# Performance work log

Hardware: AMD Instinct MI355X
Metric: run time of the kernel (lower is better)

Reference implementation:

```python
import jax, jax.numpy as jnp
import numpy as np
from jax import lax

B, OBS, E, H = 65536, 20, 64, 64


def setup_inputs() -> dict:
    key = jax.random.key(0)
    ks = jax.random.split(key, 13)
    s = 0.1
    inp = {
        "obs_traj": jax.random.normal(ks[0], (B, OBS, 2), jnp.float32),
        "W_emb": jax.random.normal(ks[1], (E, 2), jnp.float32) * s,
        "b_emb": jax.random.normal(ks[2], (E,), jnp.float32) * s,
        "Wih_e": jax.random.normal(ks[3], (4 * H, E), jnp.float32) * s,
        "Whh_e": jax.random.normal(ks[4], (4 * H, H), jnp.float32) * s,
        "bih_e": jax.random.normal(ks[5], (4 * H,), jnp.float32) * s,
        "bhh_e": jax.random.normal(ks[6], (4 * H,), jnp.float32) * s,
        "Wih_d": jax.random.normal(ks[7], (4 * H, E), jnp.float32) * s,
        "Whh_d": jax.random.normal(ks[8], (4 * H, H), jnp.float32) * s,
        "bih_d": jax.random.normal(ks[9], (4 * H,), jnp.float32) * s,
        "bhh_d": jax.random.normal(ks[10], (4 * H,), jnp.float32) * s,
        "W_fc": jax.random.normal(ks[11], (2, H), jnp.float32) * s,
        "b_fc": jax.random.normal(ks[12], (2,), jnp.float32) * s,
        "pred_len": 12,
    }
    return inp


def _lstm_step(x, h, c, Wih, Whh, b):
    # PyTorch LSTM gate order: i, f, g, o
    g = x @ Wih.T + h @ Whh.T + b  # [B, 4H]
    i, f, gg, o = jnp.split(g, 4, axis=-1)
    c2 = jax.nn.sigmoid(f) * c + jax.nn.sigmoid(i) * jnp.tanh(gg)
    h2 = jax.nn.sigmoid(o) * jnp.tanh(c2)
    return h2, c2


def reference(obs_traj, W_emb, b_emb, Wih_e, Whh_e, bih_e, bhh_e,
              Wih_d, Whh_d, bih_d, bhh_d, W_fc, b_fc, pred_len):
    bsz = obs_traj.shape[0]
    dt = obs_traj.dtype
    # Encoder: embed all observed steps at once, then scan the LSTM over time.
    emb = jax.nn.relu(obs_traj @ W_emb.T + b_emb)  # [B, OBS, E]
    b_e = bih_e + bhh_e
    h0 = jnp.zeros((bsz, H), dt)
    c0 = jnp.zeros((bsz, H), dt)

    def enc_step(carry, x_t):
        h, c = carry
        h, c = _lstm_step(x_t, h, c, Wih_e, Whh_e, b_e)
        return (h, c), None

    (h, c), _ = lax.scan(enc_step, (h0, c0), jnp.swapaxes(emb, 0, 1))

    b_d = bih_d + bhh_d
    dec_in = jax.nn.relu(obs_traj[:, -1, :] @ W_emb.T + b_emb)  # [B, E]

    def dec_step(carry, _):
        h, c, x = carry
        h, c = _lstm_step(x, h, c, Wih_d, Whh_d, b_d)
        pred = h @ W_fc.T + b_fc  # [B, 2]
        nxt = jax.nn.relu(pred @ W_emb.T + b_emb)
        return (h, c, nxt), pred

    _, preds = lax.scan(dec_step, (h, c, dec_in), None, length=pred_len)
    return jnp.swapaxes(preds, 0, 1)  # [B, pred_len, 2]
```

## Files before the change

### kernel.cpp

```cpp
#include <hip/hip_runtime.h>

typedef __bf16 bf16x8 __attribute__((ext_vector_type(8)));
typedef __bf16 bf16x4 __attribute__((ext_vector_type(4)));
typedef float  f32x4  __attribute__((ext_vector_type(4)));
typedef float  f32x2  __attribute__((ext_vector_type(2)));

constexpr int BATCH = 65536;
constexpr int OBS   = 20;
constexpr int PRED  = 12;
constexpr int BT    = 128;
constexpr int AST   = 136;

constexpr float SIO = -1.4426950408889634f;
constexpr float SG  =  2.8853900817779268f;

__device__ __forceinline__ float exp2_(float x) { return __builtin_amdgcn_exp2f(x); }
__device__ __forceinline__ float rcp_(float x)  { return __builtin_amdgcn_rcpf(x); }

struct SmallW {
    float  bcomb_e[256];
    float  bcomb_d[256];
    float4 embc[64];
    float  wfc[128];
    float  bfc[2];
};

__global__ __launch_bounds__(256, 2)
void vanilla_lstm(const float* __restrict__ obs,
                  const float* __restrict__ W_emb, const float* __restrict__ b_emb,
                  const float* __restrict__ Wih_e, const float* __restrict__ Whh_e,
                  const float* __restrict__ bih_e, const float* __restrict__ bhh_e,
                  const float* __restrict__ Wih_d, const float* __restrict__ Whh_d,
                  const float* __restrict__ bih_d, const float* __restrict__ bhh_d,
                  const float* __restrict__ W_fc,  const float* __restrict__ b_fc,
                  float* __restrict__ out)
{
    __shared__ __align__(16) __bf16 As[BT * AST];
    __shared__ __align__(16) float  pred_s[BT * 2];
    __shared__ SmallW sw;

    const int tid  = threadIdx.x;
    const int wv   = tid >> 6;
    const int lane = tid & 63;
    const int m    = lane & 15;
    const int q    = lane >> 4;
    const int wblk = wv * 16;
    const size_t gRow0 = (size_t)blockIdx.x * BT;

    sw.bcomb_e[tid] = bih_e[tid] + bhh_e[tid];
    sw.bcomb_d[tid] = bih_d[tid] + bhh_d[tid];
    if (tid < 64)  sw.embc[tid] = make_float4(W_emb[2 * tid], W_emb[2 * tid + 1], b_emb[tid], 0.f);
    if (tid < 128) sw.wfc[tid]  = W_fc[tid];
    if (tid < 2)   sw.bfc[tid]  = b_fc[tid];

    {
        uint4 z; z.x = z.y = z.z = z.w = 0u;
        uint4* p = (uint4*)As;
        constexpr int NV = BT * AST * 2 / 16;
        #pragma unroll
        for (int i = 0; i < NV / 256; ++i) p[tid + i * 256] = z;
        if (tid < (NV % 256)) p[tid + (NV / 256) * 256] = z;
    }

    bf16x8 bfr[4][4];
    auto load_bfr = [&](const float* Wih, const float* Whh) {
        #pragma unroll
        for (int c = 0; c < 4; ++c) {
            const float sc = (c == 2) ? SG : SIO;
            const int n = c * 64 + wblk + m;
            #pragma unroll
            for (int kt = 0; kt < 4; ++kt) {
                const float* s = (kt < 2) ? (Wih + n * 64 + kt * 32 + q * 8)
                                          : (Whh + n * 64 + (kt - 2) * 32 + q * 8);
                float4 a = *(const float4*)s;
                float4 b = *(const float4*)(s + 4);
                bf16x8 v;
                v[0] = (__bf16)(sc * a.x); v[1] = (__bf16)(sc * a.y);
                v[2] = (__bf16)(sc * a.z); v[3] = (__bf16)(sc * a.w);
                v[4] = (__bf16)(sc * b.x); v[5] = (__bf16)(sc * b.y);
                v[6] = (__bf16)(sc * b.z); v[7] = (__bf16)(sc * b.w);
                bfr[c][kt] = v;
            }
        }
    };
    load_bfr(Wih_e, Whh_e);

    f32x4 cst[8];
    #pragma unroll
    for (int i = 0; i < 8; ++i) cst[i] = f32x4{0.f, 0.f, 0.f, 0.f};

    __syncthreads();

    f32x4 bias4[4];
    auto load_bias = [&](const float* bc) {
        #pragma unroll
        for (int c = 0; c < 4; ++c) {
            const float sc = (c == 2) ? SG : SIO;
            f32x4 b = *(const f32x4*)&bc[c * 64 + wblk + q * 4];
            bias4[c] = f32x4{sc * b[0], sc * b[1], sc * b[2], sc * b[3]};
        }
    };
    load_bias(sw.bcomb_e);

    f32x4 acc[2][2][4];

    auto gemm_sub = [&](int chunk, int half) {
        #pragma unroll
        for (int nt = 0; nt < 2; ++nt)
            #pragma unroll
            for (int c = 0; c < 4; ++c)
                acc[half][nt][c] = bias4[c];
        #pragma unroll
        for (int kt = 0; kt < 4; ++kt) {
            bf16x8 af[2];
            #pragma unroll
            for (int nt = 0; nt < 2; ++nt)
                af[nt] = *(const bf16x8*)&As[(chunk * 64 + (half * 2 + nt) * 16 + m) * AST + kt * 32 + q * 8];
            #pragma unroll
            for (int nt = 0; nt < 2; ++nt)
                #pragma unroll
                for (int c = 0; c < 4; ++c)
                    acc[half][nt][c] = __builtin_amdgcn_mfma_f32_16x16x32_bf16(
                        bfr[c][kt], af[nt], acc[half][nt][c], 0, 0, 0);
        }
    };

    auto update_sub = [&](int chunk, int half) {
        #pragma unroll
        for (int nt = 0; nt < 2; ++nt) {
            const int idx = chunk * 4 + half * 2 + nt;
            const int row = chunk * 64 + (half * 2 + nt) * 16 + m;
            f32x4 ci = cst[idx];
            bf16x4 h4;
            #pragma unroll
            for (int r = 0; r < 4; ++r) {
                const float gi = acc[half][nt][0][r];
                const float gf = acc[half][nt][1][r];
                const float gg = acc[half][nt][2][r];
                const float go = acc[half][nt][3][r];
                const float Ef = exp2_(gf);
                const float a  = ci[r] * rcp_(1.0f + Ef);
                const float Ei = exp2_(gi);
                const float Eg = exp2_(fminf(fmaxf(gg, -80.f), 80.f));
                const float d1 = 1.0f + Ei;
                const float r1 = rcp_(fmaf(d1, Eg, d1));
                const float cN = fmaf(Eg - 1.0f, r1, a);
                const float Eo = exp2_(go);
                const float Ec = exp2_(fminf(fmaxf(cN * SG, -80.f), 80.f));
                const float d2 = 1.0f + Eo;
                const float r2 = rcp_(fmaf(d2, Ec, d2));
                const float h  = (Ec - 1.0f) * r2;
                ci[r] = cN;
                h4[r] = (__bf16)h;
            }
            cst[idx] = ci;
            *(bf16x4*)&As[row * AST + 64 + wblk + q * 4] = h4;
        }
    };

    auto emb_row = [&](int row, float o0, float o1) {
        #pragma unroll
        for (int h8 = 0; h8 < 2; ++h8) {
            bf16x8 v;
            #pragma unroll
            for (int j = 0; j < 8; ++j) {
                float4 wc = sw.embc[wblk + h8 * 8 + j];
                v[j] = (__bf16)fmaxf(fmaf(o0, wc.x, fmaf(o1, wc.y, wc.z)), 0.f);
            }
            *(bf16x8*)&As[row * AST + wblk + h8 * 8] = v;
        }
    };

    const float* obr0 = obs + (gRow0 + lane) * (OBS * 2);
    const float* obr1 = obs + (gRow0 + 64 + lane) * (OBS * 2);

    {
        f32x2 o0 = *(const f32x2*)obr0;
        f32x2 o1 = *(const f32x2*)obr1;
        emb_row(lane, o0[0], o0[1]);
        emb_row(64 + lane, o1[0], o1[1]);
    }
    __syncthreads();
    gemm_sub(0, 0);
    gemm_sub(0, 1);

    for (int t = 0; t < OBS; ++t) {
        __syncthreads();
        f32x2 on0{0.f, 0.f};
        if (t + 1 < OBS) on0 = *(const f32x2*)(obr0 + (t + 1) * 2);
        update_sub(0, 0);
        gemm_sub(1, 0);
        update_sub(0, 1);
        gemm_sub(1, 1);
        if (t + 1 < OBS) emb_row(lane, on0[0], on0[1]);
        __syncthreads();
        f32x2 on1{0.f, 0.f};
        if (t + 1 < OBS) on1 = *(const f32x2*)(obr1 + (t + 1) * 2);
        update_sub(1, 0);
        if (t + 1 < OBS) gemm_sub(0, 0);
        update_sub(1, 1);
        if (t + 1 < OBS) {
            gemm_sub(0, 1);
            emb_row(64 + lane, on1[0], on1[1]);
        }
    }

    load_bfr(Wih_d, Whh_d);
    load_bias(sw.bcomb_d);
    gemm_sub(0, 0);
    gemm_sub(0, 1);

    auto pred_phase = [&](int chunk, int td) {
        const int prow = chunk * 64 + (tid >> 2);
        const int comp = (tid >> 1) & 1, half = tid & 1;
        const int cb = half * 32;
        float p = 0.f;
        #pragma unroll
        for (int e8 = 0; e8 < 4; ++e8) {
            bf16x8 hv = *(const bf16x8*)&As[prow * AST + 64 + cb + e8 * 8];
            f32x4 w0 = *(const f32x4*)&sw.wfc[comp * 64 + cb + e8 * 8];
            f32x4 w1 = *(const f32x4*)&sw.wfc[comp * 64 + cb + e8 * 8 + 4];
            p += (float)hv[0] * w0[0] + (float)hv[1] * w0[1] + (float)hv[2] * w0[2] + (float)hv[3] * w0[3]
               + (float)hv[4] * w1[0] + (float)hv[5] * w1[1] + (float)hv[6] * w1[2] + (float)hv[7] * w1[3];
        }
        p += __shfl_xor(p, 1, 64);
        if (half == 0) {
            p += sw.bfc[comp];
            pred_s[prow * 2 + comp] = p;
            out[((gRow0 + prow) * PRED + td) * 2 + comp] = p;
        }
    };
    auto emb_dec = [&](int chunk) {
        const int row = chunk * 64 + lane;
        f32x2 pv = *(const f32x2*)&pred_s[row * 2];
        emb_row(row, pv[0], pv[1]);
    };

    for (int td = 0; td < PRED; ++td) {
        __syncthreads();
        update_sub(0, 0);
        gemm_sub(1, 0);
        update_sub(0, 1);
        gemm_sub(1, 1);
        __syncthreads();
        update_sub(1, 0);
        update_sub(1, 1);
        pred_phase(0, td);
        __syncthreads();
        pred_phase(1, td);
        if (td + 1 < PRED) emb_dec(0);
        __syncthreads();
        if (td + 1 < PRED) {
            emb_dec(1);
            gemm_sub(0, 0);
            gemm_sub(0, 1);
        }
    }
}

extern "C" void kernel_launch(void* const* d_in, const int* in_sizes, int n_in,
                              void* d_out, int out_size, void* d_ws, size_t ws_size,
                              hipStream_t stream) {
    (void)in_sizes; (void)n_in; (void)d_ws; (void)ws_size; (void)out_size;
    const float* obs   = (const float*)d_in[0];
    const float* W_emb = (const float*)d_in[1];
    const float* b_emb = (const float*)d_in[2];
    const float* Wih_e = (const float*)d_in[3];
    const float* Whh_e = (const float*)d_in[4];
    const float* bih_e = (const float*)d_in[5];
    const float* bhh_e = (const float*)d_in[6];
    const float* Wih_d = (const float*)d_in[7];
    const float* Whh_d = (const float*)d_in[8];
    const float* bih_d = (const float*)d_in[9];
    const float* bhh_d = (const float*)d_in[10];
    const float* W_fc  = (const float*)d_in[11];
    const float* b_fc  = (const float*)d_in[12];
    float* o = (float*)d_out;

    dim3 grid(BATCH / BT), block(256);
    hipLaunchKernelGGL(vanilla_lstm, grid, block, 0, stream,
                       obs, W_emb, b_emb, Wih_e, Whh_e, bih_e, bhh_e,
                       Wih_d, Whh_d, bih_d, bhh_d, W_fc, b_fc, o);
}
```

Before: 285.2 us.

## Halve batch tile to 64 rows and raise occupancy to three blocks per CU

```diff
diff --git a/kernel.cpp b/kernel.cpp
--- a/kernel.cpp
+++ b/kernel.cpp
@@ -8,7 +8,7 @@
 constexpr int BATCH = 65536;
 constexpr int OBS   = 20;
 constexpr int PRED  = 12;
-constexpr int BT    = 128;
+constexpr int BT    = 64;
 constexpr int AST   = 136;
 
 constexpr float SIO = -1.4426950408889634f;
@@ -18,14 +18,14 @@
 __device__ __forceinline__ float rcp_(float x)  { return __builtin_amdgcn_rcpf(x); }
 
 struct SmallW {
-    float  bcomb_e[256];
-    float  bcomb_d[256];
+    float  biasf_e[256];
+    float  biasf_d[256];
     float4 embc[64];
     float  wfc[128];
     float  bfc[2];
 };
 
-__global__ __launch_bounds__(256, 2)
+__global__ __launch_bounds__(256, 3)
 void vanilla_lstm(const float* __restrict__ obs,
                   const float* __restrict__ W_emb, const float* __restrict__ b_emb,
                   const float* __restrict__ Wih_e, const float* __restrict__ Whh_e,
@@ -47,8 +47,13 @@
     const int wblk = wv * 16;
     const size_t gRow0 = (size_t)blockIdx.x * BT;
 
-    sw.bcomb_e[tid] = bih_e[tid] + bhh_e[tid];
-    sw.bcomb_d[tid] = bih_d[tid] + bhh_d[tid];
+    {
+        const int wv_ = tid >> 6, c_ = (tid >> 4) & 3, qr = tid & 15;
+        const int g = c_ * 64 + wv_ * 16 + qr;
+        const float sc = (c_ == 2) ? SG : SIO;
+        sw.biasf_e[tid] = sc * (bih_e[g] + bhh_e[g]);
+        sw.biasf_d[tid] = sc * (bih_d[g] + bhh_d[g]);
+    }
     if (tid < 64)  sw.embc[tid] = make_float4(W_emb[2 * tid], W_emb[2 * tid + 1], b_emb[tid], 0.f);
     if (tid < 128) sw.wfc[tid]  = W_fc[tid];
     if (tid < 2)   sw.bfc[tid]  = b_fc[tid];
@@ -85,68 +90,58 @@
     };
     load_bfr(Wih_e, Whh_e);
 
-    f32x4 cst[8];
+    f32x4 cst[4];
     #pragma unroll
-    for (int i = 0; i < 8; ++i) cst[i] = f32x4{0.f, 0.f, 0.f, 0.f};
+    for (int i = 0; i < 4; ++i) cst[i] = f32x4{0.f, 0.f, 0.f, 0.f};
 
     __syncthreads();
 
-    f32x4 bias4[4];
-    auto load_bias = [&](const float* bc) {
+    f32x4 acc[2][2][4];
+
+    auto gemm = [&](int chunk, const float* bfrag) {
         #pragma unroll
         for (int c = 0; c < 4; ++c) {
-            const float sc = (c == 2) ? SG : SIO;
-            f32x4 b = *(const f32x4*)&bc[c * 64 + wblk + q * 4];
-            bias4[c] = f32x4{sc * b[0], sc * b[1], sc * b[2], sc * b[3]};
-        }
-    };
-    load_bias(sw.bcomb_e);
-
-    f32x4 acc[2][2][4];
-
-    auto gemm_sub = [&](int chunk, int half) {
-        #pragma unroll
-        for (int nt = 0; nt < 2; ++nt)
-            #pragma unroll
-            for (int c = 0; c < 4; ++c)
-                acc[half][nt][c] = bias4[c];
+            f32x4 b = *(const f32x4*)&bfrag[(wv * 4 + c) * 16 + q * 4];
+            acc[chunk][0][c] = b;
+            acc[chunk][1][c] = b;
+        }
         #pragma unroll
         for (int kt = 0; kt < 4; ++kt) {
             bf16x8 af[2];
             #pragma unroll
-            for (int nt = 0; nt < 2; ++nt)
-                af[nt] = *(const bf16x8*)&As[(chunk * 64 + (half * 2 + nt) * 16 + m) * AST + kt * 32 + q * 8];
-            #pragma unroll
-            for (int nt = 0; nt < 2; ++nt)
+            for (int sub = 0; sub < 2; ++sub)
+                af[sub] = *(const bf16x8*)&As[(chunk * 32 + sub * 16 + m) * AST + kt * 32 + q * 8];
+            #pragma unroll
+            for (int sub = 0; sub < 2; ++sub)
                 #pragma unroll
                 for (int c = 0; c < 4; ++c)
-                    acc[half][nt][c] = __builtin_amdgcn_mfma_f32_16x16x32_bf16(
-                        bfr[c][kt], af[nt], acc[half][nt][c], 0, 0, 0);
-        }
-    };
-
-    auto update_sub = [&](int chunk, int half) {
-        #pragma unroll
-        for (int nt = 0; nt < 2; ++nt) {
-            const int idx = chunk * 4 + half * 2 + nt;
-            const int row = chunk * 64 + (half * 2 + nt) * 16 + m;
+                    acc[chunk][sub][c] = __builtin_amdgcn_mfma_f32_16x16x32_bf16(
+                        bfr[c][kt], af[sub], acc[chunk][sub][c], 0, 0, 0);
+        }
+    };
+
+    auto update = [&](int chunk) {
+        #pragma unroll
+        for (int sub = 0; sub < 2; ++sub) {
+            const int idx = chunk * 2 + sub;
+            const int row = chunk * 32 + sub * 16 + m;
             f32x4 ci = cst[idx];
             bf16x4 h4;
             #pragma unroll
             for (int r = 0; r < 4; ++r) {
-                const float gi = acc[half][nt][0][r];
-                const float gf = acc[half][nt][1][r];
-                const float gg = acc[half][nt][2][r];
-                const float go = acc[half][nt][3][r];
+                const float gi = acc[chunk][sub][0][r];
+                const float gf = acc[chunk][sub][1][r];
+                const float gg = acc[chunk][sub][2][r];
+                const float go = acc[chunk][sub][3][r];
                 const float Ef = exp2_(gf);
                 const float a  = ci[r] * rcp_(1.0f + Ef);
                 const float Ei = exp2_(gi);
-                const float Eg = exp2_(fminf(fmaxf(gg, -80.f), 80.f));
+                const float Eg = exp2_(gg);
                 const float d1 = 1.0f + Ei;
                 const float r1 = rcp_(fmaf(d1, Eg, d1));
                 const float cN = fmaf(Eg - 1.0f, r1, a);
                 const float Eo = exp2_(go);
-                const float Ec = exp2_(fminf(fmaxf(cN * SG, -80.f), 80.f));
+                const float Ec = exp2_(cN * SG);
                 const float d2 = 1.0f + Eo;
                 const float r2 = rcp_(fmaf(d2, Ec, d2));
                 const float h  = (Ec - 1.0f) * r2;
@@ -158,93 +153,83 @@
         }
     };
 
-    auto emb_row = [&](int row, float o0, float o1) {
-        #pragma unroll
-        for (int h8 = 0; h8 < 2; ++h8) {
-            bf16x8 v;
-            #pragma unroll
-            for (int j = 0; j < 8; ++j) {
-                float4 wc = sw.embc[wblk + h8 * 8 + j];
-                v[j] = (__bf16)fmaxf(fmaf(o0, wc.x, fmaf(o1, wc.y, wc.z)), 0.f);
-            }
-            *(bf16x8*)&As[row * AST + wblk + h8 * 8] = v;
-        }
-    };
-
-    const float* obr0 = obs + (gRow0 + lane) * (OBS * 2);
-    const float* obr1 = obs + (gRow0 + 64 + lane) * (OBS * 2);
+    auto emb_chunk = [&](int chunk, float o0, float o1) {
+        const int row = chunk * 32 + (lane & 31);
+        const int h8  = lane >> 5;
+        bf16x8 v;
+        #pragma unroll
+        for (int j = 0; j < 8; ++j) {
+            float4 wc = sw.embc[wblk + h8 * 8 + j];
+            v[j] = (__bf16)fmaxf(fmaf(o0, wc.x, fmaf(o1, wc.y, wc.z)), 0.f);
+        }
+        *(bf16x8*)&As[row * AST + wblk + h8 * 8] = v;
+    };
+
+    const float* obr = obs + (gRow0 + (lane & 31)) * (OBS * 2);
 
     {
-        f32x2 o0 = *(const f32x2*)obr0;
-        f32x2 o1 = *(const f32x2*)obr1;
-        emb_row(lane, o0[0], o0[1]);
-        emb_row(64 + lane, o1[0], o1[1]);
+        f32x2 o0 = *(const f32x2*)obr;
+        f32x2 o1 = *(const f32x2*)(obr + 32 * (OBS * 2));
+        emb_chunk(0, o0[0], o0[1]);
+        emb_chunk(1, o1[0], o1[1]);
     }
     __syncthreads();
-    gemm_sub(0, 0);
-    gemm_sub(0, 1);
+    gemm(0, sw.biasf_e);
 
     for (int t = 0; t < OBS; ++t) {
         __syncthreads();
         f32x2 on0{0.f, 0.f};
-        if (t + 1 < OBS) on0 = *(const f32x2*)(obr0 + (t + 1) * 2);
-        update_sub(0, 0);
-        gemm_sub(1, 0);
-        update_sub(0, 1);
-        gemm_sub(1, 1);
-        if (t + 1 < OBS) emb_row(lane, on0[0], on0[1]);
+        if (t + 1 < OBS) on0 = *(const f32x2*)(obr + (t + 1) * 2);
+        update(0);
+        gemm(1, sw.biasf_e);
+        if (t + 1 < OBS) emb_chunk(0, on0[0], on0[1]);
         __syncthreads();
         f32x2 on1{0.f, 0.f};
-        if (t + 1 < OBS) on1 = *(const f32x2*)(obr1 + (t + 1) * 2);
-        update_sub(1, 0);
-        if (t + 1 < OBS) gemm_sub(0, 0);
-        update_sub(1, 1);
+        if (t + 1 < OBS) on1 = *(const f32x2*)(obr + 32 * (OBS * 2) + (t + 1) * 2);
+        update(1);
         if (t + 1 < OBS) {
-            gemm_sub(0, 1);
-            emb_row(64 + lane, on1[0], on1[1]);
+            gemm(0, sw.biasf_e);
+            emb_chunk(1, on1[0], on1[1]);
         }
     }
 
     load_bfr(Wih_d, Whh_d);
-    load_bias(sw.bcomb_d);
-    gemm_sub(0, 0);
-    gemm_sub(0, 1);
+    gemm(0, sw.biasf_d);
 
     auto pred_phase = [&](int chunk, int td) {
-        const int prow = chunk * 64 + (tid >> 2);
-        const int comp = (tid >> 1) & 1, half = tid & 1;
-        const int cb = half * 32;
-        float p = 0.f;
-        #pragma unroll
-        for (int e8 = 0; e8 < 4; ++e8) {
-            bf16x8 hv = *(const bf16x8*)&As[prow * AST + 64 + cb + e8 * 8];
-            f32x4 w0 = *(const f32x4*)&sw.wfc[comp * 64 + cb + e8 * 8];
-            f32x4 w1 = *(const f32x4*)&sw.wfc[comp * 64 + cb + e8 * 8 + 4];
-            p += (float)hv[0] * w0[0] + (float)hv[1] * w0[1] + (float)hv[2] * w0[2] + (float)hv[3] * w0[3]
-               + (float)hv[4] * w1[0] + (float)hv[5] * w1[1] + (float)hv[6] * w1[2] + (float)hv[7] * w1[3];
-        }
+        const int row  = chunk * 32 + (tid >> 3);
+        const int comp = (tid >> 2) & 1;
+        const int seg  = tid & 3;
+        bf16x8 h0 = *(const bf16x8*)&As[row * AST + 64 + seg * 16];
+        bf16x8 h1 = *(const bf16x8*)&As[row * AST + 64 + seg * 16 + 8];
+        f32x4 w0 = *(const f32x4*)&sw.wfc[comp * 64 + seg * 16];
+        f32x4 w1 = *(const f32x4*)&sw.wfc[comp * 64 + seg * 16 + 4];
+        f32x4 w2 = *(const f32x4*)&sw.wfc[comp * 64 + seg * 16 + 8];
+        f32x4 w3 = *(const f32x4*)&sw.wfc[comp * 64 + seg * 16 + 12];
+        float p = (float)h0[0] * w0[0] + (float)h0[1] * w0[1] + (float)h0[2] * w0[2] + (float)h0[3] * w0[3]
+                + (float)h0[4] * w1[0] + (float)h0[5] * w1[1] + (float)h0[6] * w1[2] + (float)h0[7] * w1[3]
+                + (float)h1[0] * w2[0] + (float)h1[1] * w2[1] + (float)h1[2] * w2[2] + (float)h1[3] * w2[3]
+                + (float)h1[4] * w3[0] + (float)h1[5] * w3[1] + (float)h1[6] * w3[2] + (float)h1[7] * w3[3];
         p += __shfl_xor(p, 1, 64);
-        if (half == 0) {
+        p += __shfl_xor(p, 2, 64);
+        if (seg == 0) {
             p += sw.bfc[comp];
-            pred_s[prow * 2 + comp] = p;
-            out[((gRow0 + prow) * PRED + td) * 2 + comp] = p;
+            pred_s[row * 2 + comp] = p;
+            out[((gRow0 + row) * PRED + td) * 2 + comp] = p;
         }
     };
     auto emb_dec = [&](int chunk) {
-        const int row = chunk * 64 + lane;
+        const int row = chunk * 32 + (lane & 31);
         f32x2 pv = *(const f32x2*)&pred_s[row * 2];
-        emb_row(row, pv[0], pv[1]);
+        emb_chunk(chunk, pv[0], pv[1]);
     };
 
     for (int td = 0; td < PRED; ++td) {
         __syncthreads();
-        update_sub(0, 0);
-        gemm_sub(1, 0);
-        update_sub(0, 1);
-        gemm_sub(1, 1);
-        __syncthreads();
-        update_sub(1, 0);
-        update_sub(1, 1);
+        update(0);
+        gemm(1, sw.biasf_d);
+        __syncthreads();
+        update(1);
         pred_phase(0, td);
         __syncthreads();
         pred_phase(1, td);
@@ -252,8 +237,7 @@
         __syncthreads();
         if (td + 1 < PRED) {
             emb_dec(1);
-            gemm_sub(0, 0);
-            gemm_sub(0, 1);
+            gemm(0, sw.biasf_d);
         }
     }
 }
```

New measurement: 302.2 us. 5.9% more time.
